# Performance work log

Hardware: AMD Instinct MI355X
Metric: run time of the kernel (lower is better)

## Reference

```python
import jax, jax.numpy as jnp
import numpy as np

RADIUS = 1
WIN = 2 * RADIUS + 1


def setup_inputs() -> dict:
    key = jax.random.key(0)
    k1, k2 = jax.random.split(key)
    shape = (2, 64, 80, 80, 80)  # (b, c, d, h, w)
    x = jax.random.normal(k1, shape, dtype=jnp.float32)
    y = jax.random.normal(k2, shape, dtype=jnp.float32)
    return {"x": x, "y": y}


def reference(x, y):
    b, c, d, h, w = x.shape
    # zero-pad y by RADIUS on all three spatial dims
    y_padded = jnp.pad(
        y, ((0, 0), (0, 0), (RADIUS, RADIUS), (RADIUS, RADIUS), (RADIUS, RADIUS))
    )
    corrs = []
    for dz in range(WIN):
        for dy in range(WIN):
            for dx in range(WIN):
                y_win = y_padded[:, :, dz:dz + d, dy:dy + h, dx:dx + w]
                # channel-summed correlation for this offset -> [b, d, h, w]
                corrs.append(jnp.sum(x * y_win, axis=1))
    corr = jnp.stack(corrs, axis=1)
    return corr * (c ** -0.5)
```

## Files before the change

### kernel.cpp

```cpp
#include <hip/hip_runtime.h>

#define NT 320
#define TZ 4
#define TH 4
#define PZ 6
#define PH 6
#define STR 84
#define PROWS (PZ*PH)
#define NSLOT (PROWS*20)

__device__ __forceinline__ void store_f4u(float* p, float4 v) {
    __builtin_memcpy(p, &v, 16);
}

__device__ __forceinline__ void block_sync_lds() {
    asm volatile("s_waitcnt lgkmcnt(0)" ::: "memory");
    __builtin_amdgcn_s_barrier();
}

__global__ __launch_bounds__(NT)
void wincorr_kernel(const float* __restrict__ x, const float* __restrict__ y,
                    float* __restrict__ out)
{
    __shared__ __align__(16) float buf[2][PROWS * STR];

    const long long plane = 512000;
    const int tid = threadIdx.x;
    const int twi = tid % 20;
    const int th  = (tid / 20) % TH;
    const int tz  = tid / 80;

    const int zt = blockIdx.x, ht = blockIdx.y, b = blockIdx.z;
    const int z0 = zt * TZ, h0 = ht * TH;
    const int gz = z0 + tz, gh = h0 + th, wb = 4 * twi;

    const float* xb = x + (long long)b * 64 * plane;
    const float* yb = y + (long long)b * 64 * plane;
    const long long xoff = (long long)gz * 6400 + gh * 80 + wb;
    const long long xoffm = xoff - (wb > 0 ? 1 : 0);
    const long long xoffp = xoff + (wb < 76 ? 4 : 3);

    int  goff[3], loff[3];
    bool val[3];
    const bool inr2 = (tid + 2 * NT) < NSLOT;
#pragma unroll
    for (int k = 0; k < 3; ++k) {
        int s   = tid + k * NT;
        int row = s / 20, col = s % 20;
        int pz = row / PH, py = row % PH;
        int yz = z0 - 1 + pz, yh = h0 - 1 + py;
        bool ok = (s < NSLOT) && ((unsigned)yz < 80u) && ((unsigned)yh < 80u);
        val[k]  = ok;
        goff[k] = yz * 6400 + yh * 80 + 4 * col;
        loff[k] = row * STR + 4 * col;
    }

    float4 acc[27];
#pragma unroll
    for (int o = 0; o < 27; ++o) acc[o] = make_float4(0.f, 0.f, 0.f, 0.f);

    const float4 zero4 = make_float4(0.f, 0.f, 0.f, 0.f);

    auto compute = [&](const float* B, float4 xv, float xml, float xpr) {
#pragma unroll
        for (int dz = 0; dz < 3; ++dz) {
#pragma unroll
            for (int dy = 0; dy < 3; ++dy) {
                const float4 r = *(const float4*)(B + ((tz + dz) * PH + (th + dy)) * STR + wb);
                const int o = (dz * 3 + dy) * 3;
                acc[o].x   += xv.y * r.x; acc[o].y   += xv.z * r.y;
                acc[o].z   += xv.w * r.z; acc[o].w   += xpr  * r.w;
                acc[o+1].x += xv.x * r.x; acc[o+1].y += xv.y * r.y;
                acc[o+1].z += xv.z * r.z; acc[o+1].w += xv.w * r.w;
                acc[o+2].x += xml  * r.x; acc[o+2].y += xv.x * r.y;
                acc[o+2].z += xv.y * r.z; acc[o+2].w += xv.z * r.w;
            }
        }
    };

    {
        const float* yc = yb;
        float4 t0 = val[0] ? *(const float4*)(yc + goff[0]) : zero4;
        float4 t1 = val[1] ? *(const float4*)(yc + goff[1]) : zero4;
        float4 t2 = val[2] ? *(const float4*)(yc + goff[2]) : zero4;
        *(float4*)(&buf[0][loff[0]]) = t0;
        *(float4*)(&buf[0][loff[1]]) = t1;
        if (inr2) *(float4*)(&buf[0][loff[2]]) = t2;
    }
    float4 yA0, yA1, yA2;
    {
        const float* yc = yb + plane;
        yA0 = val[0] ? *(const float4*)(yc + goff[0]) : zero4;
        yA1 = val[1] ? *(const float4*)(yc + goff[1]) : zero4;
        yA2 = val[2] ? *(const float4*)(yc + goff[2]) : zero4;
    }
    float4 xvA = *(const float4*)(xb + xoff);
    float  xmA = xb[xoffm];
    float  xpA = xb[xoffp];

    block_sync_lds();

#pragma unroll 2
    for (int c = 0; c < 62; ++c) {
        float* W = (float*)buf[(c + 1) & 1];
        *(float4*)(W + loff[0]) = yA0;
        *(float4*)(W + loff[1]) = yA1;
        if (inr2) *(float4*)(W + loff[2]) = yA2;

        const float* yc = yb + (long long)(c + 2) * plane;
        float4 yB0 = val[0] ? *(const float4*)(yc + goff[0]) : zero4;
        float4 yB1 = val[1] ? *(const float4*)(yc + goff[1]) : zero4;
        float4 yB2 = val[2] ? *(const float4*)(yc + goff[2]) : zero4;

        const float* xcp = xb + (long long)(c + 1) * plane;
        float4 xvB = *(const float4*)(xcp + xoff);
        float  xmB = xcp[xoffm];
        float  xpB = xcp[xoffp];

        compute(buf[c & 1], xvA, xmA, xpA);

        block_sync_lds();
        xvA = xvB; xmA = xmB; xpA = xpB;
        yA0 = yB0; yA1 = yB1; yA2 = yB2;
    }

    {
        float* W = (float*)buf[1];
        *(float4*)(W + loff[0]) = yA0;
        *(float4*)(W + loff[1]) = yA1;
        if (inr2) *(float4*)(W + loff[2]) = yA2;

        const float* xcp = xb + 63LL * plane;
        float4 xvB = *(const float4*)(xcp + xoff);
        float  xmB = xcp[xoffm];
        float  xpB = xcp[xoffp];

        compute(buf[0], xvA, xmA, xpA);

        block_sync_lds();
        xvA = xvB; xmA = xmB; xpA = xpB;
    }
    compute(buf[1], xvA, xmA, xpA);

    float* ob = out + (long long)b * 27 * plane + xoff;
#pragma unroll
    for (int dz = 0; dz < 3; ++dz) {
#pragma unroll
        for (int dy = 0; dy < 3; ++dy) {
            const int o = (dz * 3 + dy) * 3;
            float4 a0 = acc[o], a1 = acc[o+1], a2 = acc[o+2];
            a0.x *= 0.125f; a0.y *= 0.125f; a0.z *= 0.125f; a0.w *= 0.125f;
            a1.x *= 0.125f; a1.y *= 0.125f; a1.z *= 0.125f; a1.w *= 0.125f;
            a2.x *= 0.125f; a2.y *= 0.125f; a2.z *= 0.125f; a2.w *= 0.125f;
            float* p0 = ob + (long long)(o    ) * plane;
            float* p1 = ob + (long long)(o + 1) * plane;
            float* p2 = ob + (long long)(o + 2) * plane;
            if (twi < 19) store_f4u(p0 + 1, a0);
            else { p0[1] = a0.x; p0[2] = a0.y; p0[3] = a0.z; }
            if (twi == 0) p0[0] = 0.f;
            *(float4*)p1 = a1;
            if (twi > 0) store_f4u(p2 - 1, a2);
            else { p2[0] = a2.y; p2[1] = a2.z; p2[2] = a2.w; }
            if (twi == 19) p2[3] = 0.f;
        }
    }
}

extern "C" void kernel_launch(void* const* d_in, const int* in_sizes, int n_in,
                              void* d_out, int out_size, void* d_ws, size_t ws_size,
                              hipStream_t stream) {
    const float* x = (const float*)d_in[0];
    const float* y = (const float*)d_in[1];
    float* out = (float*)d_out;

    dim3 grid(80 / TZ, 80 / TH, 2);
    dim3 block(NT);
    wincorr_kernel<<<grid, block, 0, stream>>>(x, y, out);
}
```

Baseline: 623.5 us.

## Deepen channel pipeline to triple LDS buffer with two-ahead register prefetch

Switches from double to triple LDS buffering and prefetches y and x two channels ahead in registers instead of one, so more global loads stay in flight during compute. Loads become unconditional by clamping addresses to valid rows, and out-of-range halo slots are zero-filled once in every buffer rather than each iteration. The cost is extra registers for the second prefetch stage, which may lower occupancy given the 27 float4 accumulators, plus more LDS per block.

```diff
diff --git a/kernel.cpp b/kernel.cpp
--- a/kernel.cpp
+++ b/kernel.cpp
@@ -22,7 +22,7 @@
 void wincorr_kernel(const float* __restrict__ x, const float* __restrict__ y,
                     float* __restrict__ out)
 {
-    __shared__ __align__(16) float buf[2][PROWS * STR];
+    __shared__ __align__(16) float buf[3][PROWS * STR];
 
     const long long plane = 512000;
     const int tid = threadIdx.x;
@@ -42,24 +42,30 @@
 
     int  goff[3], loff[3];
     bool val[3];
-    const bool inr2 = (tid + 2 * NT) < NSLOT;
 #pragma unroll
     for (int k = 0; k < 3; ++k) {
-        int s   = tid + k * NT;
-        int row = s / 20, col = s % 20;
-        int pz = row / PH, py = row % PH;
+        int s    = tid + k * NT;
+        int row  = s / 20, col = s % 20;
+        bool inslot = (s < NSLOT);
+        int rowc = inslot ? row : (PROWS - 1);
+        int pz = rowc / PH, py = rowc % PH;
         int yz = z0 - 1 + pz, yh = h0 - 1 + py;
-        bool ok = (s < NSLOT) && ((unsigned)yz < 80u) && ((unsigned)yh < 80u);
-        val[k]  = ok;
-        goff[k] = yz * 6400 + yh * 80 + 4 * col;
+        bool inrange = ((unsigned)yz < 80u) && ((unsigned)yh < 80u);
+        val[k]  = inslot && inrange;
+        int yzc = min(max(yz, 0), 79), yhc = min(max(yh, 0), 79);
+        goff[k] = yzc * 6400 + yhc * 80 + 4 * col;
         loff[k] = row * STR + 4 * col;
+        if (inslot && !inrange) {
+            const float4 z4 = make_float4(0.f, 0.f, 0.f, 0.f);
+            *(float4*)(&buf[0][loff[k]]) = z4;
+            *(float4*)(&buf[1][loff[k]]) = z4;
+            *(float4*)(&buf[2][loff[k]]) = z4;
+        }
     }
 
     float4 acc[27];
 #pragma unroll
     for (int o = 0; o < 27; ++o) acc[o] = make_float4(0.f, 0.f, 0.f, 0.f);
-
-    const float4 zero4 = make_float4(0.f, 0.f, 0.f, 0.f);
 
     auto compute = [&](const float* B, float4 xv, float xml, float xpr) {
 #pragma unroll
@@ -79,68 +85,100 @@
     };
 
     {
-        const float* yc = yb;
-        float4 t0 = val[0] ? *(const float4*)(yc + goff[0]) : zero4;
-        float4 t1 = val[1] ? *(const float4*)(yc + goff[1]) : zero4;
-        float4 t2 = val[2] ? *(const float4*)(yc + goff[2]) : zero4;
-        *(float4*)(&buf[0][loff[0]]) = t0;
-        *(float4*)(&buf[0][loff[1]]) = t1;
-        if (inr2) *(float4*)(&buf[0][loff[2]]) = t2;
-    }
-    float4 yA0, yA1, yA2;
-    {
-        const float* yc = yb + plane;
-        yA0 = val[0] ? *(const float4*)(yc + goff[0]) : zero4;
-        yA1 = val[1] ? *(const float4*)(yc + goff[1]) : zero4;
-        yA2 = val[2] ? *(const float4*)(yc + goff[2]) : zero4;
+        float4 t0 = *(const float4*)(yb + goff[0]);
+        float4 t1 = *(const float4*)(yb + goff[1]);
+        float4 t2 = *(const float4*)(yb + goff[2]);
+        if (val[0]) *(float4*)(&buf[0][loff[0]]) = t0;
+        if (val[1]) *(float4*)(&buf[0][loff[1]]) = t1;
+        if (val[2]) *(float4*)(&buf[0][loff[2]]) = t2;
+    }
+    float4 yA0, yA1, yA2, yB0, yB1, yB2;
+    {
+        const float* y1 = yb + plane;
+        yA0 = *(const float4*)(y1 + goff[0]);
+        yA1 = *(const float4*)(y1 + goff[1]);
+        yA2 = *(const float4*)(y1 + goff[2]);
+        const float* y2 = yb + 2 * plane;
+        yB0 = *(const float4*)(y2 + goff[0]);
+        yB1 = *(const float4*)(y2 + goff[1]);
+        yB2 = *(const float4*)(y2 + goff[2]);
     }
     float4 xvA = *(const float4*)(xb + xoff);
-    float  xmA = xb[xoffm];
-    float  xpA = xb[xoffp];
+    float  xmA = xb[xoffm], xpA = xb[xoffp];
+    const float* x1 = xb + plane;
+    float4 xvB = *(const float4*)(x1 + xoff);
+    float  xmB = x1[xoffm], xpB = x1[xoffp];
 
     block_sync_lds();
 
-#pragma unroll 2
-    for (int c = 0; c < 62; ++c) {
-        float* W = (float*)buf[(c + 1) & 1];
-        *(float4*)(W + loff[0]) = yA0;
-        *(float4*)(W + loff[1]) = yA1;
-        if (inr2) *(float4*)(W + loff[2]) = yA2;
-
-        const float* yc = yb + (long long)(c + 2) * plane;
-        float4 yB0 = val[0] ? *(const float4*)(yc + goff[0]) : zero4;
-        float4 yB1 = val[1] ? *(const float4*)(yc + goff[1]) : zero4;
-        float4 yB2 = val[2] ? *(const float4*)(yc + goff[2]) : zero4;
-
-        const float* xcp = xb + (long long)(c + 1) * plane;
-        float4 xvB = *(const float4*)(xcp + xoff);
-        float  xmB = xcp[xoffm];
-        float  xpB = xcp[xoffp];
-
-        compute(buf[c & 1], xvA, xmA, xpA);
-
-        block_sync_lds();
-        xvA = xvB; xmA = xmB; xpA = xpB;
+#pragma unroll 3
+    for (int c = 0; c < 60; ++c) {
+        float* W = (float*)buf[(c + 1) % 3];
+        if (val[0]) *(float4*)(W + loff[0]) = yA0;
+        if (val[1]) *(float4*)(W + loff[1]) = yA1;
+        if (val[2]) *(float4*)(W + loff[2]) = yA2;
+
+        const float* yc = yb + (long long)(c + 3) * plane;
+        float4 yC0 = *(const float4*)(yc + goff[0]);
+        float4 yC1 = *(const float4*)(yc + goff[1]);
+        float4 yC2 = *(const float4*)(yc + goff[2]);
+
+        const float* xcp = xb + (long long)(c + 2) * plane;
+        float4 xvC = *(const float4*)(xcp + xoff);
+        float  xmC = xcp[xoffm], xpC = xcp[xoffp];
+
+        compute(buf[c % 3], xvA, xmA, xpA);
+        block_sync_lds();
+
         yA0 = yB0; yA1 = yB1; yA2 = yB2;
+        yB0 = yC0; yB1 = yC1; yB2 = yC2;
+        xvA = xvB; xmA = xmB; xpA = xpB;
+        xvB = xvC; xmB = xmC; xpB = xpC;
     }
 
     {
         float* W = (float*)buf[1];
-        *(float4*)(W + loff[0]) = yA0;
-        *(float4*)(W + loff[1]) = yA1;
-        if (inr2) *(float4*)(W + loff[2]) = yA2;
-
+        if (val[0]) *(float4*)(W + loff[0]) = yA0;
+        if (val[1]) *(float4*)(W + loff[1]) = yA1;
+        if (val[2]) *(float4*)(W + loff[2]) = yA2;
+        const float* yc = yb + 63LL * plane;
+        float4 yC0 = *(const float4*)(yc + goff[0]);
+        float4 yC1 = *(const float4*)(yc + goff[1]);
+        float4 yC2 = *(const float4*)(yc + goff[2]);
+        const float* xcp = xb + 62LL * plane;
+        float4 xvC = *(const float4*)(xcp + xoff);
+        float  xmC = xcp[xoffm], xpC = xcp[xoffp];
+        compute(buf[0], xvA, xmA, xpA);
+        block_sync_lds();
+        yA0 = yB0; yA1 = yB1; yA2 = yB2;
+        yB0 = yC0; yB1 = yC1; yB2 = yC2;
+        xvA = xvB; xmA = xmB; xpA = xpB;
+        xvB = xvC; xmB = xmC; xpB = xpC;
+    }
+    {
+        float* W = (float*)buf[2];
+        if (val[0]) *(float4*)(W + loff[0]) = yA0;
+        if (val[1]) *(float4*)(W + loff[1]) = yA1;
+        if (val[2]) *(float4*)(W + loff[2]) = yA2;
         const float* xcp = xb + 63LL * plane;
-        float4 xvB = *(const float4*)(xcp + xoff);
-        float  xmB = xcp[xoffm];
-        float  xpB = xcp[xoffp];
-
-        compute(buf[0], xvA, xmA, xpA);
-
-        block_sync_lds();
-        xvA = xvB; xmA = xmB; xpA = xpB;
-    }
-    compute(buf[1], xvA, xmA, xpA);
+        float4 xvC = *(const float4*)(xcp + xoff);
+        float  xmC = xcp[xoffm], xpC = xcp[xoffp];
+        compute(buf[1], xvA, xmA, xpA);
+        block_sync_lds();
+        yA0 = yB0; yA1 = yB1; yA2 = yB2;
+        xvA = xvB; xmA = xmB; xpA = xpB;
+        xvB = xvC; xmB = xmC; xpB = xpC;
+    }
+    {
+        float* W = (float*)buf[0];
+        if (val[0]) *(float4*)(W + loff[0]) = yA0;
+        if (val[1]) *(float4*)(W + loff[1]) = yA1;
+        if (val[2]) *(float4*)(W + loff[2]) = yA2;
+        compute(buf[2], xvA, xmA, xpA);
+        block_sync_lds();
+        xvA = xvB; xmA = xmB; xpA = xpB;
+    }
+    compute(buf[0], xvA, xmA, xpA);
 
     float* ob = out + (long long)b * 27 * plane + xoff;
 #pragma unroll
```

Result: slower. 881.8 us (+41.4%).
